# Performance work log

Measured on AMD Instinct MI355X. Metric: run time of the kernel, lower is better.

Reference implementation:

```python
import jax, jax.numpy as jnp
import numpy as np

N_AGENT = 32768   # number of agent (dst) nodes
MAX_NBRS = 16     # fixed neighbor count per agent (pad target)
N_NBR = N_AGENT * MAX_NBRS   # nbr (src) nodes
E = N_AGENT * MAX_NBRS       # 1hop edges (grouped by dst)
F_NBR, F_AGENT, F_HOP = 32, 32, 8
H = 128           # critic_hidden_size
N_POW = 4         # n_pow_opts


def _lin(key, fin, fout):
    return jax.random.normal(key, (fin, fout), jnp.float32) / np.sqrt(fin)


def setup_inputs() -> dict:
    key = jax.random.key(0)
    ks = jax.random.split(key, 12)
    return {
        "feat_nbr": jax.random.normal(ks[0], (N_NBR, F_NBR), jnp.float32),
        "feat_agent": jax.random.normal(ks[1], (N_AGENT, F_AGENT), jnp.float32),
        "edge_feat": jax.random.normal(ks[2], (E, F_HOP), jnp.float32),
        "h": jnp.zeros((N_AGENT, H), jnp.float32),
        # NodeGNBlock '1hop': message MLP + update MLP
        "W_msg": _lin(ks[3], F_NBR + F_HOP, H), "b_msg": jnp.zeros((H,), jnp.float32),
        "W_upd": _lin(ks[4], H + F_AGENT, H), "b_upd": jnp.zeros((H,), jnp.float32),
        # RnnLayer: GRUCell(H, H)
        "W_x": _lin(ks[5], H, 3 * H), "W_h": _lin(ks[6], H, 3 * H),
        "b_ih": jnp.zeros((3 * H,), jnp.float32), "b_hh": jnp.zeros((3 * H,), jnp.float32),
        # EdgeGNBlock f_out: edge MLP -> per-edge q over power options, plus agent head
        "W_e1": _lin(ks[7], F_NBR + H + F_HOP, H), "b_e1": jnp.zeros((H,), jnp.float32),
        "W_e2": _lin(ks[8], H, N_POW), "b_e2": jnp.zeros((N_POW,), jnp.float32),
        "W_a": _lin(ks[9], 2 * H, 1), "b_a": jnp.zeros((1,), jnp.float32),
        # graph: each agent has exactly MAX_NBRS incident edges, grouped by dst
        "src_idx": jax.random.randint(ks[10], (E,), 0, N_NBR),
        "dst_idx": jnp.repeat(jnp.arange(N_AGENT), MAX_NBRS),
    }


def reference(feat_nbr, feat_agent, edge_feat, h,
              W_msg, b_msg, W_upd, b_upd,
              W_x, W_h, b_ih, b_hh,
              W_e1, b_e1, W_e2, b_e2, W_a, b_a,
              src_idx, dst_idx):
    act = jax.nn.relu
    # --- NodeGNBlock '1hop': edge message -> sum-aggregate -> node update ---
    m = act(jnp.concatenate([feat_nbr[src_idx], edge_feat], axis=1) @ W_msg + b_msg)  # [E,H]
    agg = jax.ops.segment_sum(m, dst_idx, num_segments=N_AGENT, indices_are_sorted=True)  # [N,H]
    x = act(jnp.concatenate([agg, feat_agent], axis=1) @ W_upd + b_upd)  # [N,H]
    # --- RnnLayer: GRUCell step; output x == new hidden ---
    gi = x @ W_x + b_ih
    gh = h @ W_h + b_hh
    ir, iz, inn = jnp.split(gi, 3, axis=1)
    hr, hz, hn = jnp.split(gh, 3, axis=1)
    r = jax.nn.sigmoid(ir + hr)
    z = jax.nn.sigmoid(iz + hz)
    n = jnp.tanh(inn + r * hn)
    h_new = (1.0 - z) * n + z * h  # [N,H]
    # --- EdgeGNBlock f_out: per-edge q-values + per-agent scalar ---
    ze = act(jnp.concatenate([feat_nbr[src_idx], h_new[dst_idx], edge_feat], axis=1) @ W_e1 + b_e1)  # [E,H]
    nbr_out = ze @ W_e2 + b_e2  # [E, N_POW]
    agg2 = jax.ops.segment_sum(ze, dst_idx, num_segments=N_AGENT, indices_are_sorted=True)
    agent_out = jnp.concatenate([agg2, h_new], axis=1) @ W_a + b_a  # [N,1]
    # --- pad_edge_output: edges grouped by dst with fixed degree -> reshape ---
    padded_nbr_out = nbr_out.reshape(N_AGENT, MAX_NBRS * N_POW)
    q_vals = jnp.concatenate([padded_nbr_out, agent_out], axis=1)  # [N, MAX_NBRS*N_POW+1]
    return q_vals, h_new
```

## Files before the change

kernel.cpp:

```cpp
#include <hip/hip_runtime.h>

typedef _Float16 half_t;
typedef half_t half8 __attribute__((ext_vector_type(8)));
typedef half_t half4 __attribute__((ext_vector_type(4)));
typedef float f32x4 __attribute__((ext_vector_type(4)));

#define NAGENT 32768
#define MAXN   16
#define HD     128
#define QCOLS  65
#define QN     (NAGENT * QCOLS)
#define AGB    16
#define EPB    (AGB * MAXN)

#define O_WMT   0
#define O_WE1E  8192
#define O_WE1H  16384
#define O_WUPD  32768
#define O_WX    53248
#define O_WH    102400
#define W_TOTAL 151552

#define MFMA(a, b, c) __builtin_amdgcn_mfma_f32_16x16x32_f16((a), (b), (c), 0, 0, 0)

__global__ void prep_weights(const float* __restrict__ W_msg, const float* __restrict__ W_upd,
                             const float* __restrict__ W_x, const float* __restrict__ W_h,
                             const float* __restrict__ W_e1, half_t* __restrict__ ws) {
    int i = blockIdx.x * 256 + threadIdx.x;
    if (i >= W_TOTAL) return;
    float v; int dst;
    if (i < 8192) {
        int k = i >> 7, n = i & 127;
        v = (k < 40) ? W_msg[k * HD + n] : 0.f;
        dst = O_WMT + n * 64 + k;
    } else if (i < 16384) {
        int j = i - 8192; int k = j >> 7, n = j & 127;
        v = (k < 32) ? W_e1[k * HD + n] : (k < 40 ? W_e1[(160 + k - 32) * HD + n] : 0.f);
        dst = O_WE1E + n * 64 + k;
    } else if (i < 32768) {
        int j = i - 16384; int k = j >> 7, n = j & 127;
        v = W_e1[(32 + k) * HD + n];
        dst = O_WE1H + n * 128 + k;
    } else if (i < 53248) {
        int j = i - 32768; int k = j >> 7, n = j & 127;
        v = W_upd[k * HD + n];
        dst = O_WUPD + n * 160 + k;
    } else if (i < 102400) {
        int j = i - 53248; int k = j / 384, n = j - k * 384;
        v = W_x[k * 384 + n];
        dst = O_WX + n * 128 + k;
    } else {
        int j = i - 102400; int k = j / 384, n = j - k * 384;
        v = W_h[k * 384 + n];
        dst = O_WH + n * 128 + k;
    }
    ws[dst] = (half_t)v;
}

__device__ __forceinline__ half8 ldB(const half_t* __restrict__ WT, int kstride, int n0, int k0, int l) {
    return *(const half8*)(WT + (size_t)(n0 + (l & 15)) * kstride + k0 + ((l >> 4) * 8));
}
__device__ __forceinline__ half4 cvt4(float4 v) {
    return (half4){(half_t)v.x, (half_t)v.y, (half_t)v.z, (half_t)v.w};
}
__device__ __forceinline__ half8 cvt8(float4 a, float4 b) {
    return (half8){(half_t)a.x, (half_t)a.y, (half_t)a.z, (half_t)a.w,
                   (half_t)b.x, (half_t)b.y, (half_t)b.z, (half_t)b.w};
}
__device__ __forceinline__ float sigm(float x) { return 1.f / (1.f + __expf(-x)); }
__device__ __forceinline__ float tanh_fast(float x) { return 1.f - 2.f / (__expf(2.f * x) + 1.f); }

__global__ __launch_bounds__(256, 4) void fused_gnn(
    const float* __restrict__ feat_nbr, const float* __restrict__ feat_agent,
    const float* __restrict__ edge_feat, const float* __restrict__ h_in,
    const float* __restrict__ b_msg, const float* __restrict__ b_upd,
    const float* __restrict__ b_ih, const float* __restrict__ b_hh,
    const float* __restrict__ b_e1, const float* __restrict__ W_e2,
    const float* __restrict__ b_e2, const float* __restrict__ W_a,
    const float* __restrict__ b_a, const int* __restrict__ src_idx,
    const half_t* __restrict__ ws, float* __restrict__ out)
{
    const int t = threadIdx.x;
    const int w = t >> 6;
    const int l = t & 63;
    const int l16 = l & 15, q = l >> 4;
    const int a0 = blockIdx.x * AGB;
    const int be = blockIdx.x * EPB;

    const half_t* wmT   = ws + O_WMT;
    const half_t* we1eT = ws + O_WE1E;
    const half_t* we1hT = ws + O_WE1H;
    const half_t* wupdT = ws + O_WUPD;
    const half_t* wxT   = ws + O_WX;
    const half_t* whT   = ws + O_WH;

    __shared__ half_t A2[AGB][168];
    __shared__ half_t x_lds[AGB][136];
    __shared__ half_t h_lds[AGB][136];
    __shared__ half_t hn_lds[AGB][136];
    __shared__ half_t che[AGB][136];
    __shared__ int    srcs[EPB];

    const half8 hz = {0, 0, 0, 0, 0, 0, 0, 0};

    srcs[t] = src_idx[be + t];
    #pragma unroll
    for (int i = 0; i < 2; ++i) {
        int g = t + 256 * i; int r = g >> 5, c = g & 31;
        float4 v = ((const float4*)(h_in + (size_t)(a0 + r) * HD))[c];
        *(half4*)&h_lds[r][c * 4] = cvt4(v);
    }
    if (t < 128) {
        int r = t >> 3, p = t & 7;
        float4 v = ((const float4*)(feat_agent + (size_t)(a0 + r) * 32))[p];
        *(half4*)&A2[r][128 + p * 4] = cvt4(v);
    }
    __syncthreads();

    #pragma unroll
    for (int mt = 0; mt < 4; ++mt) {
        const int al = w * 4 + mt;
        const int arow = al * 16 + l16;
        const float* fr = feat_nbr + (size_t)srcs[arow] * 32 + q * 8;
        half8 af0 = cvt8(*(const float4*)fr, *(const float4*)(fr + 4));
        half8 af1 = hz;
        if (q == 0) {
            const float* er = edge_feat + (size_t)(be + arow) * 8;
            af1 = cvt8(*(const float4*)er, *(const float4*)(er + 4));
        }
        #pragma unroll
        for (int nc = 0; nc < 4; ++nc) {
            const int n0 = nc * 32;
            f32x4 c0 = {0.f, 0.f, 0.f, 0.f}, c1 = {0.f, 0.f, 0.f, 0.f};
            c0 = MFMA(af0, ldB(wmT, 64, n0, 0, l), c0);
            c0 = MFMA(af1, ldB(wmT, 64, n0, 32, l), c0);
            c1 = MFMA(af0, ldB(wmT, 64, n0 + 16, 0, l), c1);
            c1 = MFMA(af1, ldB(wmT, 64, n0 + 16, 32, l), c1);
            float bm0 = b_msg[n0 + l16], bm1 = b_msg[n0 + 16 + l16];
            float s0 = 0.f, s1 = 0.f;
            #pragma unroll
            for (int r = 0; r < 4; ++r) {
                s0 += fmaxf(c0[r] + bm0, 0.f);
                s1 += fmaxf(c1[r] + bm1, 0.f);
            }
            s0 += __shfl_xor(s0, 16); s0 += __shfl_xor(s0, 32);
            s1 += __shfl_xor(s1, 16); s1 += __shfl_xor(s1, 32);
            if (l < 16) {
                A2[al][n0 + l] = (half_t)s0;
                A2[al][n0 + 16 + l] = (half_t)s1;
            }
        }
    }
    __syncthreads();

    {
        half8 af[5];
        #pragma unroll
        for (int k = 0; k < 5; ++k) af[k] = *(const half8*)&A2[l16][k * 32 + q * 8];
        #pragma unroll
        for (int s = 0; s < 2; ++s) {
            const int n0 = (w * 2 + s) * 16;
            f32x4 c = {0.f, 0.f, 0.f, 0.f};
            #pragma unroll
            for (int k = 0; k < 5; ++k) c = MFMA(af[k], ldB(wupdT, 160, n0, k * 32, l), c);
            float bu = b_upd[n0 + l16];
            #pragma unroll
            for (int r = 0; r < 4; ++r)
                x_lds[q * 4 + r][n0 + l16] = (half_t)fmaxf(c[r] + bu, 0.f);
        }
    }
    __syncthreads();

    {
        half8 ax[4], ah[4];
        #pragma unroll
        for (int k = 0; k < 4; ++k) {
            ax[k] = *(const half8*)&x_lds[l16][k * 32 + q * 8];
            ah[k] = *(const half8*)&h_lds[l16][k * 32 + q * 8];
        }
        #pragma unroll
        for (int s = 0; s < 2; ++s) {
            const int colb = w * 32 + s * 16;
            f32x4 gi[3], gh[3];
            #pragma unroll
            for (int g = 0; g < 3; ++g) {
                const int n0 = g * 128 + colb;
                f32x4 ci = {0.f, 0.f, 0.f, 0.f}, ch = {0.f, 0.f, 0.f, 0.f};
                #pragma unroll
                for (int k = 0; k < 4; ++k) {
                    ci = MFMA(ax[k], ldB(wxT, 128, n0, k * 32, l), ci);
                    ch = MFMA(ah[k], ldB(whT, 128, n0, k * 32, l), ch);
                }
                gi[g] = ci; gh[g] = ch;
            }
            const int col = colb + l16;
            float bi0 = b_ih[col], bi1 = b_ih[HD + col], bi2 = b_ih[2 * HD + col];
            float bh0 = b_hh[col], bh1 = b_hh[HD + col], bh2 = b_hh[2 * HD + col];
            #pragma unroll
            for (int r = 0; r < 4; ++r) {
                const int row = q * 4 + r;
                float rg = sigm(gi[0][r] + bi0 + gh[0][r] + bh0);
                float zg = sigm(gi[1][r] + bi1 + gh[1][r] + bh1);
                float ng = tanh_fast(gi[2][r] + bi2 + rg * (gh[2][r] + bh2));
                float hv = (1.f - zg) * ng + zg * (float)h_lds[row][col];
                out[QN + (size_t)(a0 + row) * HD + col] = hv;
                hn_lds[row][col] = (half_t)hv;
            }
        }
    }
    __syncthreads();

    {
        half8 an[4];
        #pragma unroll
        for (int k = 0; k < 4; ++k) an[k] = *(const half8*)&hn_lds[l16][k * 32 + q * 8];
        #pragma unroll
        for (int s = 0; s < 2; ++s) {
            const int n0 = (w * 2 + s) * 16;
            f32x4 c = {0.f, 0.f, 0.f, 0.f};
            #pragma unroll
            for (int k = 0; k < 4; ++k) c = MFMA(an[k], ldB(we1hT, 128, n0, k * 32, l), c);
            float bv = b_e1[n0 + l16];
            #pragma unroll
            for (int r = 0; r < 4; ++r)
                che[q * 4 + r][n0 + l16] = (half_t)(c[r] + bv);
        }
    }
    __syncthreads();

    {
        const float ba = b_a[0];
        #pragma unroll
        for (int mt = 0; mt < 4; ++mt) {
            const int al = w * 4 + mt;
            const int arow = al * 16 + l16;
            const float* fr = feat_nbr + (size_t)srcs[arow] * 32 + q * 8;
            half8 af0 = cvt8(*(const float4*)fr, *(const float4*)(fr + 4));
            half8 af1 = hz;
            if (q == 0) {
                const float* er = edge_feat + (size_t)(be + arow) * 8;
                af1 = cvt8(*(const float4*)er, *(const float4*)(er + 4));
            }
            float qa[4][4];
            #pragma unroll
            for (int r = 0; r < 4; ++r)
                #pragma unroll
                for (int p = 0; p < 4; ++p) qa[r][p] = 0.f;
            float wa_part = 0.f;
            #pragma unroll
            for (int nc = 0; nc < 4; ++nc) {
                const int n0 = nc * 32;
                f32x4 c0 = {0.f, 0.f, 0.f, 0.f}, c1 = {0.f, 0.f, 0.f, 0.f};
                c0 = MFMA(af0, ldB(we1eT, 64, n0, 0, l), c0);
                c0 = MFMA(af1, ldB(we1eT, 64, n0, 32, l), c0);
                c1 = MFMA(af0, ldB(we1eT, 64, n0 + 16, 0, l), c1);
                c1 = MFMA(af1, ldB(we1eT, 64, n0 + 16, 32, l), c1);
                const int col0 = n0 + l16, col1 = n0 + 16 + l16;
                float ch0 = (float)che[al][col0], ch1 = (float)che[al][col1];
                float4 w20 = *(const float4*)(W_e2 + col0 * 4);
                float4 w21 = *(const float4*)(W_e2 + col1 * 4);
                float s0 = 0.f, s1 = 0.f;
                #pragma unroll
                for (int r = 0; r < 4; ++r) {
                    float z0 = fmaxf(c0[r] + ch0, 0.f);
                    float z1 = fmaxf(c1[r] + ch1, 0.f);
                    s0 += z0; s1 += z1;
                    qa[r][0] = fmaf(z0, w20.x, fmaf(z1, w21.x, qa[r][0]));
                    qa[r][1] = fmaf(z0, w20.y, fmaf(z1, w21.y, qa[r][1]));
                    qa[r][2] = fmaf(z0, w20.z, fmaf(z1, w21.z, qa[r][2]));
                    qa[r][3] = fmaf(z0, w20.w, fmaf(z1, w21.w, qa[r][3]));
                }
                s0 += __shfl_xor(s0, 16); s0 += __shfl_xor(s0, 32);
                s1 += __shfl_xor(s1, 16); s1 += __shfl_xor(s1, 32);
                wa_part = fmaf(s0, W_a[col0], fmaf(s1, W_a[col1], wa_part));
            }
            #pragma unroll
            for (int m = 1; m <= 8; m <<= 1)
                #pragma unroll
                for (int r = 0; r < 4; ++r)
                    #pragma unroll
                    for (int p = 0; p < 4; ++p) qa[r][p] += __shfl_xor(qa[r][p], m);
            if (l16 < 4) {
                const int p = l16;
                const float bz = b_e2[p];
                #pragma unroll
                for (int r = 0; r < 4; ++r)
                    out[(size_t)(a0 + al) * QCOLS + (q * 4 + r) * 4 + p] = qa[r][p] + bz;
            }
            #pragma unroll
            for (int j = 0; j < 8; ++j) {
                const int c = l16 + 16 * j;
                wa_part = fmaf((float)hn_lds[al][c], W_a[HD + c], wa_part);
            }
            #pragma unroll
            for (int m = 1; m <= 8; m <<= 1) wa_part += __shfl_xor(wa_part, m);
            if (l == 0) out[(size_t)(a0 + al) * QCOLS + 64] = wa_part + ba;
        }
    }
}

extern "C" void kernel_launch(void* const* d_in, const int* in_sizes, int n_in,
                              void* d_out, int out_size, void* d_ws, size_t ws_size,
                              hipStream_t stream) {
    const float* feat_nbr   = (const float*)d_in[0];
    const float* feat_agent = (const float*)d_in[1];
    const float* edge_feat  = (const float*)d_in[2];
    const float* h_in       = (const float*)d_in[3];
    const float* W_msg = (const float*)d_in[4];
    const float* b_msg = (const float*)d_in[5];
    const float* W_upd = (const float*)d_in[6];
    const float* b_upd = (const float*)d_in[7];
    const float* W_x   = (const float*)d_in[8];
    const float* W_h   = (const float*)d_in[9];
    const float* b_ih  = (const float*)d_in[10];
    const float* b_hh  = (const float*)d_in[11];
    const float* W_e1  = (const float*)d_in[12];
    const float* b_e1  = (const float*)d_in[13];
    const float* W_e2  = (const float*)d_in[14];
    const float* b_e2  = (const float*)d_in[15];
    const float* W_a   = (const float*)d_in[16];
    const float* b_a   = (const float*)d_in[17];
    const int* src_idx = (const int*)d_in[18];
    half_t* ws = (half_t*)d_ws;
    float* out = (float*)d_out;

    prep_weights<<<(W_TOTAL + 255) / 256, 256, 0, stream>>>(W_msg, W_upd, W_x, W_h, W_e1, ws);
    fused_gnn<<<NAGENT / AGB, 256, 0, stream>>>(
        feat_nbr, feat_agent, edge_feat, h_in,
        b_msg, b_upd, b_ih, b_hh, b_e1,
        W_e2, b_e2, W_a, b_a, src_idx, ws, out);
}
```

Baseline: 339.3 us.

## Split fused GNN kernel into message, node and edge kernels

Breaks the single fused kernel into three launches: a message kernel that writes per-agent aggregates as half to a scratch region in the output buffer, a node-update/GRU kernel that also precomputes the edge-MLP h contribution and the h_new·W_a term, and an edge kernel that consumes them. Each kernel keeps its B weight fragments in registers and uses lower occupancy bounds. This is meant to cut per-kernel register/LDS pressure and stop reloading weights inside loops. The cost is that feat_nbr is now gathered twice across kernels and intermediates go through global memory, plus extra launch overhead.

```diff
diff --git a/kernel.cpp b/kernel.cpp
--- a/kernel.cpp
+++ b/kernel.cpp
@@ -12,6 +12,7 @@
 #define QN     (NAGENT * QCOLS)
 #define AGB    16
 #define EPB    (AGB * MAXN)
+#define QROWB  260
 
 #define O_WMT   0
 #define O_WE1E  8192
@@ -70,53 +71,35 @@
 __device__ __forceinline__ float sigm(float x) { return 1.f / (1.f + __expf(-x)); }
 __device__ __forceinline__ float tanh_fast(float x) { return 1.f - 2.f / (__expf(2.f * x) + 1.f); }
 
-__global__ __launch_bounds__(256, 4) void fused_gnn(
-    const float* __restrict__ feat_nbr, const float* __restrict__ feat_agent,
-    const float* __restrict__ edge_feat, const float* __restrict__ h_in,
-    const float* __restrict__ b_msg, const float* __restrict__ b_upd,
-    const float* __restrict__ b_ih, const float* __restrict__ b_hh,
-    const float* __restrict__ b_e1, const float* __restrict__ W_e2,
-    const float* __restrict__ b_e2, const float* __restrict__ W_a,
-    const float* __restrict__ b_a, const int* __restrict__ src_idx,
+__global__ __launch_bounds__(256, 2) void k_msg(
+    const float* __restrict__ feat_nbr, const float* __restrict__ edge_feat,
+    const float* __restrict__ b_msg, const int* __restrict__ src_idx,
     const half_t* __restrict__ ws, float* __restrict__ out)
 {
     const int t = threadIdx.x;
-    const int w = t >> 6;
-    const int l = t & 63;
+    const int w = t >> 6, l = t & 63;
     const int l16 = l & 15, q = l >> 4;
     const int a0 = blockIdx.x * AGB;
     const int be = blockIdx.x * EPB;
-
-    const half_t* wmT   = ws + O_WMT;
-    const half_t* we1eT = ws + O_WE1E;
-    const half_t* we1hT = ws + O_WE1H;
-    const half_t* wupdT = ws + O_WUPD;
-    const half_t* wxT   = ws + O_WX;
-    const half_t* whT   = ws + O_WH;
-
-    __shared__ half_t A2[AGB][168];
-    __shared__ half_t x_lds[AGB][136];
-    __shared__ half_t h_lds[AGB][136];
-    __shared__ half_t hn_lds[AGB][136];
-    __shared__ half_t che[AGB][136];
-    __shared__ int    srcs[EPB];
-
+    const half_t* wmT = ws + O_WMT;
     const half8 hz = {0, 0, 0, 0, 0, 0, 0, 0};
 
+    __shared__ int srcs[EPB];
     srcs[t] = src_idx[be + t];
-    #pragma unroll
-    for (int i = 0; i < 2; ++i) {
-        int g = t + 256 * i; int r = g >> 5, c = g & 31;
-        float4 v = ((const float4*)(h_in + (size_t)(a0 + r) * HD))[c];
-        *(half4*)&h_lds[r][c * 4] = cvt4(v);
-    }
-    if (t < 128) {
-        int r = t >> 3, p = t & 7;
-        float4 v = ((const float4*)(feat_agent + (size_t)(a0 + r) * 32))[p];
-        *(half4*)&A2[r][128 + p * 4] = cvt4(v);
-    }
-    __syncthreads();
-
+    __syncthreads();
+
+    half8 B[4][4];
+    float bm0[4], bm1[4];
+    #pragma unroll
+    for (int nc = 0; nc < 4; ++nc) {
+        const int n0 = nc * 32;
+        B[nc][0] = ldB(wmT, 64, n0, 0, l);
+        B[nc][1] = ldB(wmT, 64, n0, 32, l);
+        B[nc][2] = ldB(wmT, 64, n0 + 16, 0, l);
+        B[nc][3] = ldB(wmT, 64, n0 + 16, 32, l);
+        bm0[nc] = b_msg[n0 + l16];
+        bm1[nc] = b_msg[n0 + 16 + l16];
+    }
     #pragma unroll
     for (int mt = 0; mt < 4; ++mt) {
         const int al = w * 4 + mt;
@@ -128,28 +111,69 @@
             const float* er = edge_feat + (size_t)(be + arow) * 8;
             af1 = cvt8(*(const float4*)er, *(const float4*)(er + 4));
         }
+        half_t* arow_out = (half_t*)((char*)out + (size_t)(a0 + al) * QROWB);
         #pragma unroll
         for (int nc = 0; nc < 4; ++nc) {
-            const int n0 = nc * 32;
             f32x4 c0 = {0.f, 0.f, 0.f, 0.f}, c1 = {0.f, 0.f, 0.f, 0.f};
-            c0 = MFMA(af0, ldB(wmT, 64, n0, 0, l), c0);
-            c0 = MFMA(af1, ldB(wmT, 64, n0, 32, l), c0);
-            c1 = MFMA(af0, ldB(wmT, 64, n0 + 16, 0, l), c1);
-            c1 = MFMA(af1, ldB(wmT, 64, n0 + 16, 32, l), c1);
-            float bm0 = b_msg[n0 + l16], bm1 = b_msg[n0 + 16 + l16];
+            c0 = MFMA(af0, B[nc][0], c0);
+            c0 = MFMA(af1, B[nc][1], c0);
+            c1 = MFMA(af0, B[nc][2], c1);
+            c1 = MFMA(af1, B[nc][3], c1);
             float s0 = 0.f, s1 = 0.f;
             #pragma unroll
             for (int r = 0; r < 4; ++r) {
-                s0 += fmaxf(c0[r] + bm0, 0.f);
-                s1 += fmaxf(c1[r] + bm1, 0.f);
+                s0 += fmaxf(c0[r] + bm0[nc], 0.f);
+                s1 += fmaxf(c1[r] + bm1[nc], 0.f);
             }
             s0 += __shfl_xor(s0, 16); s0 += __shfl_xor(s0, 32);
             s1 += __shfl_xor(s1, 16); s1 += __shfl_xor(s1, 32);
             if (l < 16) {
-                A2[al][n0 + l] = (half_t)s0;
-                A2[al][n0 + 16 + l] = (half_t)s1;
-            }
-        }
+                arow_out[nc * 32 + l] = (half_t)s0;
+                arow_out[nc * 32 + 16 + l] = (half_t)s1;
+            }
+        }
+    }
+}
+
+__global__ __launch_bounds__(256, 2) void k_node(
+    const float* __restrict__ feat_agent, const float* __restrict__ h_in,
+    const float* __restrict__ b_upd, const float* __restrict__ b_ih,
+    const float* __restrict__ b_hh, const float* __restrict__ b_e1,
+    const float* __restrict__ W_a, half_t* __restrict__ ws,
+    float* __restrict__ out)
+{
+    const int t = threadIdx.x;
+    const int w = t >> 6, l = t & 63;
+    const int l16 = l & 15, q = l >> 4;
+    const int a0 = blockIdx.x * AGB;
+    const half_t* wupdT = ws + O_WUPD;
+    const half_t* wxT   = ws + O_WX;
+    const half_t* whT   = ws + O_WH;
+    const half_t* we1hT = ws + O_WE1H;
+    float* hn_wa_g = (float*)(ws + W_TOTAL);
+
+    __shared__ half_t A2[AGB][168];
+    __shared__ half_t h_lds[AGB][136];
+    __shared__ half_t x_lds[AGB][136];
+    __shared__ half_t hn_lds[AGB][136];
+    __shared__ float  hnwa[AGB];
+
+    if (t < AGB) hnwa[t] = 0.f;
+    {
+        int r = t >> 4, c = t & 15;
+        half8 v = *(const half8*)((const char*)out + (size_t)(a0 + r) * QROWB + c * 16);
+        *(half8*)&A2[r][c * 8] = v;
+    }
+    if (t < 128) {
+        int r = t >> 3, p = t & 7;
+        float4 v = ((const float4*)(feat_agent + (size_t)(a0 + r) * 32))[p];
+        *(half4*)&A2[r][128 + p * 4] = cvt4(v);
+    }
+    #pragma unroll
+    for (int i = 0; i < 2; ++i) {
+        int g = t + 256 * i; int r = g >> 5, c = g & 31;
+        float4 v = ((const float4*)(h_in + (size_t)(a0 + r) * HD))[c];
+        *(half4*)&h_lds[r][c * 4] = cvt4(v);
     }
     __syncthreads();
 
@@ -178,6 +202,7 @@
             ax[k] = *(const half8*)&x_lds[l16][k * 32 + q * 8];
             ah[k] = *(const half8*)&h_lds[l16][k * 32 + q * 8];
         }
+        float pa[4] = {0.f, 0.f, 0.f, 0.f};
         #pragma unroll
         for (int s = 0; s < 2; ++s) {
             const int colb = w * 32 + s * 16;
@@ -196,6 +221,7 @@
             const int col = colb + l16;
             float bi0 = b_ih[col], bi1 = b_ih[HD + col], bi2 = b_ih[2 * HD + col];
             float bh0 = b_hh[col], bh1 = b_hh[HD + col], bh2 = b_hh[2 * HD + col];
+            float wac = W_a[HD + col];
             #pragma unroll
             for (int r = 0; r < 4; ++r) {
                 const int row = q * 4 + r;
@@ -205,7 +231,14 @@
                 float hv = (1.f - zg) * ng + zg * (float)h_lds[row][col];
                 out[QN + (size_t)(a0 + row) * HD + col] = hv;
                 hn_lds[row][col] = (half_t)hv;
-            }
+                pa[r] = fmaf(hv, wac, pa[r]);
+            }
+        }
+        #pragma unroll
+        for (int r = 0; r < 4; ++r) {
+            #pragma unroll
+            for (int m = 1; m <= 8; m <<= 1) pa[r] += __shfl_xor(pa[r], m);
+            if (l16 == 0) atomicAdd(&hnwa[q * 4 + r], pa[r]);
         }
     }
     __syncthreads();
@@ -222,80 +255,111 @@
             for (int k = 0; k < 4; ++k) c = MFMA(an[k], ldB(we1hT, 128, n0, k * 32, l), c);
             float bv = b_e1[n0 + l16];
             #pragma unroll
-            for (int r = 0; r < 4; ++r)
-                che[q * 4 + r][n0 + l16] = (half_t)(c[r] + bv);
-        }
-    }
-    __syncthreads();
-
-    {
-        const float ba = b_a[0];
-        #pragma unroll
-        for (int mt = 0; mt < 4; ++mt) {
-            const int al = w * 4 + mt;
-            const int arow = al * 16 + l16;
-            const float* fr = feat_nbr + (size_t)srcs[arow] * 32 + q * 8;
-            half8 af0 = cvt8(*(const float4*)fr, *(const float4*)(fr + 4));
-            half8 af1 = hz;
-            if (q == 0) {
-                const float* er = edge_feat + (size_t)(be + arow) * 8;
-                af1 = cvt8(*(const float4*)er, *(const float4*)(er + 4));
-            }
-            float qa[4][4];
+            for (int r = 0; r < 4; ++r) {
+                half_t* arow_out = (half_t*)((char*)out + (size_t)(a0 + q * 4 + r) * QROWB);
+                arow_out[n0 + l16] = (half_t)(c[r] + bv);
+            }
+        }
+    }
+    if (t < AGB) hn_wa_g[a0 + t] = hnwa[t];
+}
+
+__global__ __launch_bounds__(256, 2) void k_edge(
+    const float* __restrict__ feat_nbr, const float* __restrict__ edge_feat,
+    const float* __restrict__ W_e2, const float* __restrict__ b_e2,
+    const float* __restrict__ W_a, const float* __restrict__ b_a,
+    const int* __restrict__ src_idx, const half_t* __restrict__ ws,
+    float* __restrict__ out)
+{
+    const int t = threadIdx.x;
+    const int w = t >> 6, l = t & 63;
+    const int l16 = l & 15, q = l >> 4;
+    const int a0 = blockIdx.x * AGB;
+    const int be = blockIdx.x * EPB;
+    const half_t* we1eT = ws + O_WE1E;
+    const float* hn_wa_g = (const float*)(ws + W_TOTAL);
+    const half8 hz = {0, 0, 0, 0, 0, 0, 0, 0};
+
+    __shared__ int srcs[EPB];
+    srcs[t] = src_idx[be + t];
+    __syncthreads();
+
+    half8 B[4][4];
+    float wa0[4], wa1[4];
+    #pragma unroll
+    for (int nc = 0; nc < 4; ++nc) {
+        const int n0 = nc * 32;
+        B[nc][0] = ldB(we1eT, 64, n0, 0, l);
+        B[nc][1] = ldB(we1eT, 64, n0, 32, l);
+        B[nc][2] = ldB(we1eT, 64, n0 + 16, 0, l);
+        B[nc][3] = ldB(we1eT, 64, n0 + 16, 32, l);
+        wa0[nc] = W_a[n0 + l16];
+        wa1[nc] = W_a[n0 + 16 + l16];
+    }
+    const float ba = b_a[0];
+
+    #pragma unroll
+    for (int mt = 0; mt < 4; ++mt) {
+        const int al = w * 4 + mt;
+        const int arow = al * 16 + l16;
+        const float* fr = feat_nbr + (size_t)srcs[arow] * 32 + q * 8;
+        half8 af0 = cvt8(*(const float4*)fr, *(const float4*)(fr + 4));
+        half8 af1 = hz;
+        if (q == 0) {
+            const float* er = edge_feat + (size_t)(be + arow) * 8;
+            af1 = cvt8(*(const float4*)er, *(const float4*)(er + 4));
+        }
+        const half_t* che_row = (const half_t*)((const char*)out + (size_t)(a0 + al) * QROWB);
+        float qa[4][4];
+        #pragma unroll
+        for (int r = 0; r < 4; ++r)
+            #pragma unroll
+            for (int p = 0; p < 4; ++p) qa[r][p] = 0.f;
+        float wa_part = 0.f;
+        #pragma unroll
+        for (int nc = 0; nc < 4; ++nc) {
+            const int n0 = nc * 32;
+            f32x4 c0 = {0.f, 0.f, 0.f, 0.f}, c1 = {0.f, 0.f, 0.f, 0.f};
+            c0 = MFMA(af0, B[nc][0], c0);
+            c0 = MFMA(af1, B[nc][1], c0);
+            c1 = MFMA(af0, B[nc][2], c1);
+            c1 = MFMA(af1, B[nc][3], c1);
+            const int col0 = n0 + l16, col1 = n0 + 16 + l16;
+            float ch0 = (float)che_row[col0], ch1 = (float)che_row[col1];
+            float4 w20 = *(const float4*)(W_e2 + col0 * 4);
+            float4 w21 = *(const float4*)(W_e2 + col1 * 4);
+            float s0 = 0.f, s1 = 0.f;
+            #pragma unroll
+            for (int r = 0; r < 4; ++r) {
+                float z0 = fmaxf(c0[r] + ch0, 0.f);
+                float z1 = fmaxf(c1[r] + ch1, 0.f);
+                s0 += z0; s1 += z1;
+                qa[r][0] = fmaf(z0, w20.x, fmaf(z1, w21.x, qa[r][0]));
+                qa[r][1] = fmaf(z0, w20.y, fmaf(z1, w21.y, qa[r][1]));
+                qa[r][2] = fmaf(z0, w20.z, fmaf(z1, w21.z, qa[r][2]));
+                qa[r][3] = fmaf(z0, w20.w, fmaf(z1, w21.w, qa[r][3]));
+            }
+            s0 += __shfl_xor(s0, 16); s0 += __shfl_xor(s0, 32);
+            s1 += __shfl_xor(s1, 16); s1 += __shfl_xor(s1, 32);
+            wa_part = fmaf(s0, wa0[nc], fmaf(s1, wa1[nc], wa_part));
+        }
+        #pragma unroll
+        for (int m = 1; m <= 8; m <<= 1)
             #pragma unroll
             for (int r = 0; r < 4; ++r)
                 #pragma unroll
-                for (int p = 0; p < 4; ++p) qa[r][p] = 0.f;
-            float wa_part = 0.f;
-            #pragma unroll
-            for (int nc = 0; nc < 4; ++nc) {
-                const int n0 = nc * 32;
-                f32x4 c0 = {0.f, 0.f, 0.f, 0.f}, c1 = {0.f, 0.f, 0.f, 0.f};
-                c0 = MFMA(af0, ldB(we1eT, 64, n0, 0, l), c0);
-                c0 = MFMA(af1, ldB(we1eT, 64, n0, 32, l), c0);
-                c1 = MFMA(af0, ldB(we1eT, 64, n0 + 16, 0, l), c1);
-                c1 = MFMA(af1, ldB(we1eT, 64, n0 + 16, 32, l), c1);
-                const int col0 = n0 + l16, col1 = n0 + 16 + l16;
-                float ch0 = (float)che[al][col0], ch1 = (float)che[al][col1];
-                float4 w20 = *(const float4*)(W_e2 + col0 * 4);
-                float4 w21 = *(const float4*)(W_e2 + col1 * 4);
-                float s0 = 0.f, s1 = 0.f;
-                #pragma unroll
-                for (int r = 0; r < 4; ++r) {
-                    float z0 = fmaxf(c0[r] + ch0, 0.f);
-                    float z1 = fmaxf(c1[r] + ch1, 0.f);
-                    s0 += z0; s1 += z1;
-                    qa[r][0] = fmaf(z0, w20.x, fmaf(z1, w21.x, qa[r][0]));
-                    qa[r][1] = fmaf(z0, w20.y, fmaf(z1, w21.y, qa[r][1]));
-                    qa[r][2] = fmaf(z0, w20.z, fmaf(z1, w21.z, qa[r][2]));
-                    qa[r][3] = fmaf(z0, w20.w, fmaf(z1, w21.w, qa[r][3]));
-                }
-                s0 += __shfl_xor(s0, 16); s0 += __shfl_xor(s0, 32);
-                s1 += __shfl_xor(s1, 16); s1 += __shfl_xor(s1, 32);
-                wa_part = fmaf(s0, W_a[col0], fmaf(s1, W_a[col1], wa_part));
-            }
-            #pragma unroll
-            for (int m = 1; m <= 8; m <<= 1)
-                #pragma unroll
-                for (int r = 0; r < 4; ++r)
-                    #pragma unroll
-                    for (int p = 0; p < 4; ++p) qa[r][p] += __shfl_xor(qa[r][p], m);
-            if (l16 < 4) {
-                const int p = l16;
-                const float bz = b_e2[p];
-                #pragma unroll
-                for (int r = 0; r < 4; ++r)
-                    out[(size_t)(a0 + al) * QCOLS + (q * 4 + r) * 4 + p] = qa[r][p] + bz;
-            }
-            #pragma unroll
-            for (int j = 0; j < 8; ++j) {
-                const int c = l16 + 16 * j;
-                wa_part = fmaf((float)hn_lds[al][c], W_a[HD + c], wa_part);
-            }
-            #pragma unroll
-            for (int m = 1; m <= 8; m <<= 1) wa_part += __shfl_xor(wa_part, m);
-            if (l == 0) out[(size_t)(a0 + al) * QCOLS + 64] = wa_part + ba;
-        }
+                for (int p = 0; p < 4; ++p) qa[r][p] += __shfl_xor(qa[r][p], m);
+        if (l16 < 4) {
+            const int p = l16;
+            const float bz = b_e2[p];
+            #pragma unroll
+            for (int r = 0; r < 4; ++r)
+                out[(size_t)(a0 + al) * QCOLS + (q * 4 + r) * 4 + p] = qa[r][p] + bz;
+        }
+        #pragma unroll
+        for (int m = 1; m <= 8; m <<= 1) wa_part += __shfl_xor(wa_part, m);
+        if (l == 0)
+            out[(size_t)(a0 + al) * QCOLS + 64] = wa_part + hn_wa_g[a0 + al] + ba;
     }
 }
 
@@ -323,10 +387,10 @@
     const int* src_idx = (const int*)d_in[18];
     half_t* ws = (half_t*)d_ws;
     float* out = (float*)d_out;
+    const int nblk = NAGENT / AGB;
 
     prep_weights<<<(W_TOTAL + 255) / 256, 256, 0, stream>>>(W_msg, W_upd, W_x, W_h, W_e1, ws);
-    fused_gnn<<<NAGENT / AGB, 256, 0, stream>>>(
-        feat_nbr, feat_agent, edge_feat, h_in,
-        b_msg, b_upd, b_ih, b_hh, b_e1,
-        W_e2, b_e2, W_a, b_a, src_idx, ws, out);
-}
+    k_msg<<<nblk, 256, 0, stream>>>(feat_nbr, edge_feat, b_msg, src_idx, ws, out);
+    k_node<<<nblk, 256, 0, stream>>>(feat_agent, h_in, b_upd, b_ih, b_hh, b_e1, W_a, ws, out);
+    k_edge<<<nblk, 256, 0, stream>>>(feat_nbr, edge_feat, W_e2, b_e2, W_a, b_a, src_idx, ws, out);
+}
```

Result: faster. 316.2 us (-6.8%).
